# Optimization experiments

Measured on AMD Instinct MI355X. Metric: run time of the kernel, lower is better.

Reference implementation:

```python
import jax, jax.numpy as jnp
import numpy as np

K, OUT, IN = 4, 4096, 4096
B, S = 2, 2048

def setup_inputs() -> dict:
    key = jax.random.key(0)
    k1, k2, k3 = jax.random.split(key, 3)
    x = jax.random.normal(k1, (B, S, IN), dtype=jnp.float32)
    alphas = jax.random.normal(k2, (K,), dtype=jnp.float32)
    # binary bases in {-1, +1}, stored as int8 like the torch buffer
    bases = (jax.random.randint(k3, (K, OUT, IN), 0, 2) * 2 - 1).astype(jnp.int8)
    return {"x": x, "alphas": alphas, "bases": bases}

def reference(x, alphas, bases):
    # W_q = sum_i alphas[i] * bases[i]  -> [out, in]
    W_q = jnp.einsum('k,koi->oi', alphas, bases.astype(x.dtype))
    # y = x @ W_q.T  -> [B, S, out]
    return jnp.einsum('bsi,oi->bso', x, W_q)
```

## Files before the change

### kernel.cpp

```cpp
#include <hip/hip_runtime.h>
#include <hip/hip_bf16.h>
#include <stdint.h>

#define DIM_M 4096
#define DIM_N 4096
#define DIM_K 4096
#define BASE_STRIDE (DIM_N * DIM_K)
#define NT (DIM_K / 64)

typedef __bf16 bf16x8 __attribute__((ext_vector_type(8)));
typedef float floatx4 __attribute__((ext_vector_type(4)));
typedef unsigned short ushort8 __attribute__((ext_vector_type(8)));

__device__ __forceinline__ unsigned short f2bf(float f) {
    uint32_t u = __float_as_uint(f);
    uint32_t r = (u + 0x7FFFu + ((u >> 16) & 1u)) >> 16;
    return (unsigned short)r;
}

__global__ __launch_bounds__(256) void prep_kernel(
        const int* __restrict__ bases, const float* __restrict__ alphas,
        const float* __restrict__ x,
        unsigned short* __restrict__ Wb, unsigned short* __restrict__ Xb) {
    const int bid = blockIdx.x;
    if (bid < 8192) {
        const long e = ((long)bid * 256 + threadIdx.x) * 8;
        const float a0 = alphas[0], a1 = alphas[1], a2 = alphas[2], a3 = alphas[3];
        const int4 p0 = *(const int4*)(bases + e);
        const int4 p1 = *(const int4*)(bases + e + 4);
        const int4 q0 = *(const int4*)(bases + BASE_STRIDE + e);
        const int4 q1 = *(const int4*)(bases + BASE_STRIDE + e + 4);
        const int4 r0 = *(const int4*)(bases + 2L * BASE_STRIDE + e);
        const int4 r1 = *(const int4*)(bases + 2L * BASE_STRIDE + e + 4);
        const int4 s0 = *(const int4*)(bases + 3L * BASE_STRIDE + e);
        const int4 s1 = *(const int4*)(bases + 3L * BASE_STRIDE + e + 4);
        ushort8 o;
        o[0] = f2bf(a0 * p0.x + a1 * q0.x + a2 * r0.x + a3 * s0.x);
        o[1] = f2bf(a0 * p0.y + a1 * q0.y + a2 * r0.y + a3 * s0.y);
        o[2] = f2bf(a0 * p0.z + a1 * q0.z + a2 * r0.z + a3 * s0.z);
        o[3] = f2bf(a0 * p0.w + a1 * q0.w + a2 * r0.w + a3 * s0.w);
        o[4] = f2bf(a0 * p1.x + a1 * q1.x + a2 * r1.x + a3 * s1.x);
        o[5] = f2bf(a0 * p1.y + a1 * q1.y + a2 * r1.y + a3 * s1.y);
        o[6] = f2bf(a0 * p1.z + a1 * q1.z + a2 * r1.z + a3 * s1.z);
        o[7] = f2bf(a0 * p1.w + a1 * q1.w + a2 * r1.w + a3 * s1.w);
        *(ushort8*)(Wb + e) = o;
    } else {
        const long e = ((long)(bid - 8192) * 256 + threadIdx.x) * 8;
        const float4 v0 = *(const float4*)(x + e);
        const float4 v1 = *(const float4*)(x + e + 4);
        ushort8 o;
        o[0] = f2bf(v0.x); o[1] = f2bf(v0.y); o[2] = f2bf(v0.z); o[3] = f2bf(v0.w);
        o[4] = f2bf(v1.x); o[5] = f2bf(v1.y); o[6] = f2bf(v1.z); o[7] = f2bf(v1.w);
        *(ushort8*)(Xb + e) = o;
    }
}

#define MFMA16 __builtin_amdgcn_mfma_f32_16x16x32_bf16
#define BAR()   __builtin_amdgcn_s_barrier()
#define PRIO1() __builtin_amdgcn_s_setprio(1)
#define PRIO0() __builtin_amdgcn_s_setprio(0)

__device__ __forceinline__ void stage_half(const unsigned short* __restrict__ gb,
        int grow0, int kbase, unsigned short* ld, int wave, int lane) {
#pragma unroll
    for (int r = 0; r < 2; ++r) {
        const int row = wave * 16 + r * 8 + (lane >> 3);
        const int ch  = (lane & 7) ^ (row & 7);
        const unsigned short* g = gb + (size_t)(grow0 + row) * DIM_K + kbase + ch * 8;
        unsigned short* d = ld + (wave * 16 + r * 8) * 64;
        __builtin_amdgcn_global_load_lds(
            (const __attribute__((address_space(1))) unsigned int*)((const void*)g),
            (__attribute__((address_space(3))) unsigned int*)((void*)d), 16, 0, 0);
    }
}

#define DS_A16(LD, MF, SLOT)                                                          \
    do {                                                                              \
        aR[SLOT][0] = *(const bf16x8*)((LD) + ((MF) * 16 + l15) * 64 + cko2[0]);      \
        aR[SLOT][1] = *(const bf16x8*)((LD) + ((MF) * 16 + l15) * 64 + cko2[1]);      \
    } while (0)
#define DS_B16(LD, NF, SLOT)                                                          \
    do {                                                                              \
        bR[SLOT][0] = *(const bf16x8*)((LD) + (nloc + (NF) * 16 + l15) * 64 + cko2[0]); \
        bR[SLOT][1] = *(const bf16x8*)((LD) + (nloc + (NF) * 16 + l15) * 64 + cko2[1]); \
    } while (0)
#define MMQ(MB, NB)                                                                   \
    do { _Pragma("unroll") for (int kh = 0; kh < 2; ++kh)                             \
        _Pragma("unroll") for (int n = 0; n < 2; ++n)                                 \
            _Pragma("unroll") for (int m = 0; m < 4; ++m)                             \
                acc4[(MB) + m][(NB) + n] = MFMA16(aR[m][kh], bR[(NB) + n][kh],        \
                                                  acc4[(MB) + m][(NB) + n], 0, 0, 0); \
    } while (0)

__global__ __launch_bounds__(512, 2) void gemm_bt_kernel(
        const unsigned short* __restrict__ A, const unsigned short* __restrict__ Bt,
        float* __restrict__ C) {
    __shared__ __align__(16) unsigned short lds[2][2][2][128 * 64];

    const int t = threadIdx.x;
    const int wave = t >> 6, lane = t & 63;
    const int l15 = lane & 15, l4 = lane >> 4;
    const int wm = wave >> 2;
    const int wn = wave & 3;
    const int nloc = (wn & 1) * 64;

    const int lin = blockIdx.y * gridDim.x + blockIdx.x;
    const int xcd = lin & 7, idx = lin >> 3;
    const int by = (xcd >> 1) * 4 + (idx >> 3);
    const int bx = (xcd & 1) * 8 + (idx & 7);
    const int mBase = by * 256;
    const int nBase = bx * 256;

    const unsigned short* LA0 = &lds[0][0][wm][0];
    const unsigned short* LA1 = &lds[1][0][wm][0];
    const unsigned short* LB0 = &lds[0][1][wn >> 1][0];
    const unsigned short* LB1 = &lds[1][1][wn >> 1][0];

    int cko2[2];
#pragma unroll
    for (int kh = 0; kh < 2; ++kh) cko2[kh] = ((l4 + 4 * kh) ^ (l15 & 7)) * 8;

    floatx4 acc4[8][4] = {};
    bf16x8 aR[4][2], bR[4][2];

    stage_half(A,  mBase + 0,   0,  &lds[0][0][0][0], wave, lane);
    stage_half(A,  mBase + 128, 0,  &lds[0][0][1][0], wave, lane);
    stage_half(Bt, nBase + 0,   0,  &lds[0][1][0][0], wave, lane);
    stage_half(Bt, nBase + 128, 0,  &lds[0][1][1][0], wave, lane);
    stage_half(Bt, nBase + 0,   64, &lds[1][1][0][0], wave, lane);
    stage_half(Bt, nBase + 128, 64, &lds[1][1][1][0], wave, lane);
    stage_half(A,  mBase + 0,   64, &lds[1][0][0][0], wave, lane);
    asm volatile("s_waitcnt vmcnt(6)" ::: "memory");
    BAR();
    DS_A16(LA0, 0, 0); DS_A16(LA0, 1, 1); DS_A16(LA0, 2, 2); DS_A16(LA0, 3, 3);
    DS_B16(LB0, 0, 0); DS_B16(LB0, 1, 1);

    for (int i = 0; i < NT / 2; ++i) {
        const bool more = (i < NT / 2 - 1);
        const int t1k = (2 * i + 1) * 64;
        const int t2k = (2 * i + 2) * 64;
        const int t3k = (2 * i + 3) * 64;

        DS_B16(LB0, 2, 2); DS_B16(LB0, 3, 3);
        stage_half(A, mBase + 128, t1k, &lds[1][0][1][0], wave, lane);
        PRIO1(); MMQ(0, 0); PRIO0();
        BAR();
        PRIO1(); MMQ(0, 2); PRIO0();
        DS_A16(LA0, 4, 0); DS_A16(LA0, 5, 1); DS_A16(LA0, 6, 2); DS_A16(LA0, 7, 3);
        BAR();
        if (more) stage_half(Bt, nBase + 0, t2k, &lds[0][1][0][0], wave, lane);
        PRIO1(); MMQ(4, 2); PRIO0();
        BAR();
        if (more) {
            stage_half(Bt, nBase + 128, t2k, &lds[0][1][1][0], wave, lane);
            stage_half(A,  mBase + 0,   t2k, &lds[0][0][0][0], wave, lane);
            asm volatile("s_waitcnt vmcnt(6)" ::: "memory");
        } else {
            asm volatile("s_waitcnt vmcnt(0)" ::: "memory");
        }
        BAR();
        PRIO1(); MMQ(4, 0); PRIO0();
        DS_A16(LA1, 0, 0); DS_A16(LA1, 1, 1); DS_A16(LA1, 2, 2); DS_A16(LA1, 3, 3);
        DS_B16(LB1, 0, 0); DS_B16(LB1, 1, 1);
        BAR();

        DS_B16(LB1, 2, 2); DS_B16(LB1, 3, 3);
        if (more) stage_half(A, mBase + 128, t2k, &lds[0][0][1][0], wave, lane);
        PRIO1(); MMQ(0, 0); PRIO0();
        BAR();
        PRIO1(); MMQ(0, 2); PRIO0();
        DS_A16(LA1, 4, 0); DS_A16(LA1, 5, 1); DS_A16(LA1, 6, 2); DS_A16(LA1, 7, 3);
        BAR();
        if (more) stage_half(Bt, nBase + 0, t3k, &lds[1][1][0][0], wave, lane);
        PRIO1(); MMQ(4, 2); PRIO0();
        BAR();
        if (more) {
            stage_half(Bt, nBase + 128, t3k, &lds[1][1][1][0], wave, lane);
            stage_half(A,  mBase + 0,   t3k, &lds[1][0][0][0], wave, lane);
            asm volatile("s_waitcnt vmcnt(6)" ::: "memory");
        } else {
            asm volatile("s_waitcnt vmcnt(0)" ::: "memory");
        }
        BAR();
        PRIO1(); MMQ(4, 0); PRIO0();
        if (more) {
            DS_A16(LA0, 0, 0); DS_A16(LA0, 1, 1); DS_A16(LA0, 2, 2); DS_A16(LA0, 3, 3);
            DS_B16(LB0, 0, 0); DS_B16(LB0, 1, 1);
        }
        BAR();
    }

#pragma unroll
    for (int mf = 0; mf < 8; ++mf) {
#pragma unroll
        for (int nf = 0; nf < 4; ++nf) {
#pragma unroll
            for (int r = 0; r < 4; ++r) {
                const int row = mBase + wm * 128 + mf * 16 + l4 * 4 + r;
                const int col = nBase + wn * 64 + nf * 16 + l15;
                C[(size_t)row * DIM_N + col] = acc4[mf][nf][r];
            }
        }
    }
}

__global__ __launch_bounds__(256) void naive_kernel(
        const float* __restrict__ x, const float* __restrict__ alphas,
        const int* __restrict__ bases, float* __restrict__ out) {
    const long o = (long)blockIdx.x * 256 + threadIdx.x;
    const int m = (int)(o >> 12), n = (int)(o & 4095);
    const float a0 = alphas[0], a1 = alphas[1], a2 = alphas[2], a3 = alphas[3];
    const float* xr = x + (long)m * DIM_K;
    const int* b0 = bases + (long)n * DIM_K;
    const int* b1 = b0 + BASE_STRIDE;
    const int* b2 = b1 + BASE_STRIDE;
    const int* b3 = b2 + BASE_STRIDE;
    float acc = 0.f;
    for (int i = 0; i < DIM_K; i++) {
        float w = a0 * b0[i] + a1 * b1[i] + a2 * b2[i] + a3 * b3[i];
        acc += xr[i] * w;
    }
    out[o] = acc;
}

extern "C" void kernel_launch(void* const* d_in, const int* in_sizes, int n_in,
                              void* d_out, int out_size, void* d_ws, size_t ws_size,
                              hipStream_t stream) {
    const float* x      = (const float*)d_in[0];
    const float* alphas = (const float*)d_in[1];
    const int*   bases  = (const int*)d_in[2];
    float* out = (float*)d_out;

    const size_t need = (size_t)2 * DIM_N * DIM_K + (size_t)2 * DIM_M * DIM_K;
    if (ws_size >= need) {
        unsigned short* Wb = (unsigned short*)d_ws;
        unsigned short* Xb = (unsigned short*)d_ws + (size_t)DIM_N * DIM_K;
        prep_kernel<<<16384, 256, 0, stream>>>(bases, alphas, x, Wb, Xb);
        gemm_bt_kernel<<<dim3(DIM_N / 256, DIM_M / 256), 512, 0, stream>>>(Xb, Wb, out);
    } else {
        naive_kernel<<<(DIM_M * DIM_N) / 256, 256, 0, stream>>>(x, alphas, bases, out);
    }
}
```

Baseline: 527.5 us.

## Fuse prep and GEMM into one cooperative kernel with grid sync

Replaces the two launches (the bf16 conversion prep kernel and the GEMM) with a single cooperative kernel of 256 blocks. Each block first does a grid-strided share of the W and X conversion, then hits a grid-wide barrier, then runs the same GEMM body. The goal is to remove the second launch and the gap between kernels. The price is that the prep phase now runs on only 256 blocks of 512 threads instead of 16384 small blocks, which may hurt memory-bandwidth saturation, and the grid sync adds its own overhead. If the cooperative launch fails, it falls back to the two-kernel path.

```diff
diff --git a/kernel.cpp b/kernel.cpp
--- a/kernel.cpp
+++ b/kernel.cpp
@@ -1,5 +1,6 @@
 #include <hip/hip_runtime.h>
 #include <hip/hip_bf16.h>
+#include <hip/hip_cooperative_groups.h>
 #include <stdint.h>
 
 #define DIM_M 4096
@@ -18,40 +19,51 @@
     return (unsigned short)r;
 }
 
+__device__ __forceinline__ void prep_w_unit(long e,
+        const int* __restrict__ bases, float a0, float a1, float a2, float a3,
+        unsigned short* __restrict__ Wb) {
+    const int4 p0 = *(const int4*)(bases + e);
+    const int4 p1 = *(const int4*)(bases + e + 4);
+    const int4 q0 = *(const int4*)(bases + BASE_STRIDE + e);
+    const int4 q1 = *(const int4*)(bases + BASE_STRIDE + e + 4);
+    const int4 r0 = *(const int4*)(bases + 2L * BASE_STRIDE + e);
+    const int4 r1 = *(const int4*)(bases + 2L * BASE_STRIDE + e + 4);
+    const int4 s0 = *(const int4*)(bases + 3L * BASE_STRIDE + e);
+    const int4 s1 = *(const int4*)(bases + 3L * BASE_STRIDE + e + 4);
+    ushort8 o;
+    o[0] = f2bf(a0 * p0.x + a1 * q0.x + a2 * r0.x + a3 * s0.x);
+    o[1] = f2bf(a0 * p0.y + a1 * q0.y + a2 * r0.y + a3 * s0.y);
+    o[2] = f2bf(a0 * p0.z + a1 * q0.z + a2 * r0.z + a3 * s0.z);
+    o[3] = f2bf(a0 * p0.w + a1 * q0.w + a2 * r0.w + a3 * s0.w);
+    o[4] = f2bf(a0 * p1.x + a1 * q1.x + a2 * r1.x + a3 * s1.x);
+    o[5] = f2bf(a0 * p1.y + a1 * q1.y + a2 * r1.y + a3 * s1.y);
+    o[6] = f2bf(a0 * p1.z + a1 * q1.z + a2 * r1.z + a3 * s1.z);
+    o[7] = f2bf(a0 * p1.w + a1 * q1.w + a2 * r1.w + a3 * s1.w);
+    *(ushort8*)(Wb + e) = o;
+}
+
+__device__ __forceinline__ void prep_x_unit(long e,
+        const float* __restrict__ x, unsigned short* __restrict__ Xb) {
+    const float4 v0 = *(const float4*)(x + e);
+    const float4 v1 = *(const float4*)(x + e + 4);
+    ushort8 o;
+    o[0] = f2bf(v0.x); o[1] = f2bf(v0.y); o[2] = f2bf(v0.z); o[3] = f2bf(v0.w);
+    o[4] = f2bf(v1.x); o[5] = f2bf(v1.y); o[6] = f2bf(v1.z); o[7] = f2bf(v1.w);
+    *(ushort8*)(Xb + e) = o;
+}
+
 __global__ __launch_bounds__(256) void prep_kernel(
         const int* __restrict__ bases, const float* __restrict__ alphas,
         const float* __restrict__ x,
         unsigned short* __restrict__ Wb, unsigned short* __restrict__ Xb) {
     const int bid = blockIdx.x;
+    const float a0 = alphas[0], a1 = alphas[1], a2 = alphas[2], a3 = alphas[3];
     if (bid < 8192) {
         const long e = ((long)bid * 256 + threadIdx.x) * 8;
-        const float a0 = alphas[0], a1 = alphas[1], a2 = alphas[2], a3 = alphas[3];
-        const int4 p0 = *(const int4*)(bases + e);
-        const int4 p1 = *(const int4*)(bases + e + 4);
-        const int4 q0 = *(const int4*)(bases + BASE_STRIDE + e);
-        const int4 q1 = *(const int4*)(bases + BASE_STRIDE + e + 4);
-        const int4 r0 = *(const int4*)(bases + 2L * BASE_STRIDE + e);
-        const int4 r1 = *(const int4*)(bases + 2L * BASE_STRIDE + e + 4);
-        const int4 s0 = *(const int4*)(bases + 3L * BASE_STRIDE + e);
-        const int4 s1 = *(const int4*)(bases + 3L * BASE_STRIDE + e + 4);
-        ushort8 o;
-        o[0] = f2bf(a0 * p0.x + a1 * q0.x + a2 * r0.x + a3 * s0.x);
-        o[1] = f2bf(a0 * p0.y + a1 * q0.y + a2 * r0.y + a3 * s0.y);
-        o[2] = f2bf(a0 * p0.z + a1 * q0.z + a2 * r0.z + a3 * s0.z);
-        o[3] = f2bf(a0 * p0.w + a1 * q0.w + a2 * r0.w + a3 * s0.w);
-        o[4] = f2bf(a0 * p1.x + a1 * q1.x + a2 * r1.x + a3 * s1.x);
-        o[5] = f2bf(a0 * p1.y + a1 * q1.y + a2 * r1.y + a3 * s1.y);
-        o[6] = f2bf(a0 * p1.z + a1 * q1.z + a2 * r1.z + a3 * s1.z);
-        o[7] = f2bf(a0 * p1.w + a1 * q1.w + a2 * r1.w + a3 * s1.w);
-        *(ushort8*)(Wb + e) = o;
+        prep_w_unit(e, bases, a0, a1, a2, a3, Wb);
     } else {
         const long e = ((long)(bid - 8192) * 256 + threadIdx.x) * 8;
-        const float4 v0 = *(const float4*)(x + e);
-        const float4 v1 = *(const float4*)(x + e + 4);
-        ushort8 o;
-        o[0] = f2bf(v0.x); o[1] = f2bf(v0.y); o[2] = f2bf(v0.z); o[3] = f2bf(v0.w);
-        o[4] = f2bf(v1.x); o[5] = f2bf(v1.y); o[6] = f2bf(v1.z); o[7] = f2bf(v1.w);
-        *(ushort8*)(Xb + e) = o;
+        prep_x_unit(e, x, Xb);
     }
 }
 
@@ -92,29 +104,34 @@
                                                   acc4[(MB) + m][(NB) + n], 0, 0, 0); \
     } while (0)
 
-__global__ __launch_bounds__(512, 2) void gemm_bt_kernel(
+#define L000 0
+#define L001 8192
+#define L010 16384
+#define L011 24576
+#define L100 32768
+#define L101 40960
+#define L110 49152
+#define L111 57344
+
+__device__ __forceinline__ void gemm_body(
         const unsigned short* __restrict__ A, const unsigned short* __restrict__ Bt,
-        float* __restrict__ C) {
-    __shared__ __align__(16) unsigned short lds[2][2][2][128 * 64];
-
-    const int t = threadIdx.x;
+        float* __restrict__ C, unsigned short* ldsb, int lin, int t) {
     const int wave = t >> 6, lane = t & 63;
     const int l15 = lane & 15, l4 = lane >> 4;
     const int wm = wave >> 2;
     const int wn = wave & 3;
     const int nloc = (wn & 1) * 64;
 
-    const int lin = blockIdx.y * gridDim.x + blockIdx.x;
     const int xcd = lin & 7, idx = lin >> 3;
     const int by = (xcd >> 1) * 4 + (idx >> 3);
     const int bx = (xcd & 1) * 8 + (idx & 7);
     const int mBase = by * 256;
     const int nBase = bx * 256;
 
-    const unsigned short* LA0 = &lds[0][0][wm][0];
-    const unsigned short* LA1 = &lds[1][0][wm][0];
-    const unsigned short* LB0 = &lds[0][1][wn >> 1][0];
-    const unsigned short* LB1 = &lds[1][1][wn >> 1][0];
+    const unsigned short* LA0 = ldsb + (wm ? L001 : L000);
+    const unsigned short* LA1 = ldsb + (wm ? L101 : L100);
+    const unsigned short* LB0 = ldsb + ((wn >> 1) ? L011 : L010);
+    const unsigned short* LB1 = ldsb + ((wn >> 1) ? L111 : L110);
 
     int cko2[2];
 #pragma unroll
@@ -123,13 +140,13 @@
     floatx4 acc4[8][4] = {};
     bf16x8 aR[4][2], bR[4][2];
 
-    stage_half(A,  mBase + 0,   0,  &lds[0][0][0][0], wave, lane);
-    stage_half(A,  mBase + 128, 0,  &lds[0][0][1][0], wave, lane);
-    stage_half(Bt, nBase + 0,   0,  &lds[0][1][0][0], wave, lane);
-    stage_half(Bt, nBase + 128, 0,  &lds[0][1][1][0], wave, lane);
-    stage_half(Bt, nBase + 0,   64, &lds[1][1][0][0], wave, lane);
-    stage_half(Bt, nBase + 128, 64, &lds[1][1][1][0], wave, lane);
-    stage_half(A,  mBase + 0,   64, &lds[1][0][0][0], wave, lane);
+    stage_half(A,  mBase + 0,   0,  ldsb + L000, wave, lane);
+    stage_half(A,  mBase + 128, 0,  ldsb + L001, wave, lane);
+    stage_half(Bt, nBase + 0,   0,  ldsb + L010, wave, lane);
+    stage_half(Bt, nBase + 128, 0,  ldsb + L011, wave, lane);
+    stage_half(Bt, nBase + 0,   64, ldsb + L110, wave, lane);
+    stage_half(Bt, nBase + 128, 64, ldsb + L111, wave, lane);
+    stage_half(A,  mBase + 0,   64, ldsb + L100, wave, lane);
     asm volatile("s_waitcnt vmcnt(6)" ::: "memory");
     BAR();
     DS_A16(LA0, 0, 0); DS_A16(LA0, 1, 1); DS_A16(LA0, 2, 2); DS_A16(LA0, 3, 3);
@@ -142,18 +159,18 @@
         const int t3k = (2 * i + 3) * 64;
 
         DS_B16(LB0, 2, 2); DS_B16(LB0, 3, 3);
-        stage_half(A, mBase + 128, t1k, &lds[1][0][1][0], wave, lane);
+        stage_half(A, mBase + 128, t1k, ldsb + L101, wave, lane);
         PRIO1(); MMQ(0, 0); PRIO0();
         BAR();
         PRIO1(); MMQ(0, 2); PRIO0();
         DS_A16(LA0, 4, 0); DS_A16(LA0, 5, 1); DS_A16(LA0, 6, 2); DS_A16(LA0, 7, 3);
         BAR();
-        if (more) stage_half(Bt, nBase + 0, t2k, &lds[0][1][0][0], wave, lane);
+        if (more) stage_half(Bt, nBase + 0, t2k, ldsb + L010, wave, lane);
         PRIO1(); MMQ(4, 2); PRIO0();
         BAR();
         if (more) {
-            stage_half(Bt, nBase + 128, t2k, &lds[0][1][1][0], wave, lane);
-            stage_half(A,  mBase + 0,   t2k, &lds[0][0][0][0], wave, lane);
+            stage_half(Bt, nBase + 128, t2k, ldsb + L011, wave, lane);
+            stage_half(A,  mBase + 0,   t2k, ldsb + L000, wave, lane);
             asm volatile("s_waitcnt vmcnt(6)" ::: "memory");
         } else {
             asm volatile("s_waitcnt vmcnt(0)" ::: "memory");
@@ -165,18 +182,18 @@
         BAR();
 
         DS_B16(LB1, 2, 2); DS_B16(LB1, 3, 3);
-        if (more) stage_half(A, mBase + 128, t2k, &lds[0][0][1][0], wave, lane);
+        if (more) stage_half(A, mBase + 128, t2k, ldsb + L001, wave, lane);
         PRIO1(); MMQ(0, 0); PRIO0();
         BAR();
         PRIO1(); MMQ(0, 2); PRIO0();
         DS_A16(LA1, 4, 0); DS_A16(LA1, 5, 1); DS_A16(LA1, 6, 2); DS_A16(LA1, 7, 3);
         BAR();
-        if (more) stage_half(Bt, nBase + 0, t3k, &lds[1][1][0][0], wave, lane);
+        if (more) stage_half(Bt, nBase + 0, t3k, ldsb + L110, wave, lane);
         PRIO1(); MMQ(4, 2); PRIO0();
         BAR();
         if (more) {
-            stage_half(Bt, nBase + 128, t3k, &lds[1][1][1][0], wave, lane);
-            stage_half(A,  mBase + 0,   t3k, &lds[1][0][0][0], wave, lane);
+            stage_half(Bt, nBase + 128, t3k, ldsb + L111, wave, lane);
+            stage_half(A,  mBase + 0,   t3k, ldsb + L100, wave, lane);
             asm volatile("s_waitcnt vmcnt(6)" ::: "memory");
         } else {
             asm volatile("s_waitcnt vmcnt(0)" ::: "memory");
@@ -202,6 +219,41 @@
             }
         }
     }
+}
+
+__global__ __launch_bounds__(512, 2) void gemm_bt_kernel(
+        const unsigned short* __restrict__ A, const unsigned short* __restrict__ Bt,
+        float* __restrict__ C) {
+    __shared__ __align__(16) unsigned short lds[2][2][2][128 * 64];
+    const int lin = blockIdx.y * gridDim.x + blockIdx.x;
+    gemm_body(A, Bt, C, &lds[0][0][0][0], lin, (int)threadIdx.x);
+}
+
+__global__ __launch_bounds__(512, 2) void fused_kernel(
+        const int* __restrict__ bases, const float* __restrict__ alphas,
+        const float* __restrict__ x,
+        unsigned short* __restrict__ Wb, unsigned short* __restrict__ Xb,
+        float* __restrict__ C) {
+    __shared__ __align__(16) unsigned short lds[2][2][2][128 * 64];
+
+    const int gtid = (int)blockIdx.x * 512 + (int)threadIdx.x;
+    {
+        const float a0 = alphas[0], a1 = alphas[1], a2 = alphas[2], a3 = alphas[3];
+#pragma unroll 1
+        for (int u = 0; u < 16; ++u) {
+            const long e = ((long)(u * 131072 + gtid)) * 8;
+            prep_w_unit(e, bases, a0, a1, a2, a3, Wb);
+        }
+#pragma unroll 1
+        for (int u = 0; u < 16; ++u) {
+            const long e = ((long)(u * 131072 + gtid)) * 8;
+            prep_x_unit(e, x, Xb);
+        }
+    }
+    __threadfence();
+    cooperative_groups::this_grid().sync();
+
+    gemm_body(Xb, Wb, C, &lds[0][0][0][0], (int)blockIdx.x, (int)threadIdx.x);
 }
 
 __global__ __launch_bounds__(256) void naive_kernel(
@@ -235,8 +287,18 @@
     if (ws_size >= need) {
         unsigned short* Wb = (unsigned short*)d_ws;
         unsigned short* Xb = (unsigned short*)d_ws + (size_t)DIM_N * DIM_K;
-        prep_kernel<<<16384, 256, 0, stream>>>(bases, alphas, x, Wb, Xb);
-        gemm_bt_kernel<<<dim3(DIM_N / 256, DIM_M / 256), 512, 0, stream>>>(Xb, Wb, out);
+
+        const int* b_ = bases; const float* al_ = alphas; const float* x_ = x;
+        unsigned short* wb_ = Wb; unsigned short* xb_ = Xb; float* c_ = out;
+        void* args[] = {(void*)&b_, (void*)&al_, (void*)&x_,
+                        (void*)&wb_, (void*)&xb_, (void*)&c_};
+        hipError_t rc = hipLaunchCooperativeKernel(
+            reinterpret_cast<void*>(fused_kernel), dim3(256), dim3(512),
+            args, 0, stream);
+        if (rc != hipSuccess) {
+            prep_kernel<<<16384, 256, 0, stream>>>(bases, alphas, x, Wb, Xb);
+            gemm_bt_kernel<<<dim3(DIM_N / 256, DIM_M / 256), 512, 0, stream>>>(Xb, Wb, out);
+        }
     } else {
         naive_kernel<<<(DIM_M * DIM_N) / 256, 256, 0, stream>>>(x, alphas, bases, out);
     }
```

New measurement: 648.7 us. 1.23x slower.
